# Kernel optimization log

Hardware: AMD Instinct MI355X
Metric: run time of the kernel (lower is better)

Reference implementation:

```python
import jax, jax.numpy as jnp
import numpy as np

N, S, R, M, C, CZ = 1, 128, 256, 256, 32, 128


def setup_inputs() -> dict:
    key = jax.random.key(0)
    k1, k2, k3, k4 = jax.random.split(key, 4)
    return {
        "msa_repr": jax.random.normal(k1, (N, S, R, M), dtype=jnp.float32) * 0.1,
        "left_w": jax.random.normal(k2, (M, C), dtype=jnp.float32) * 0.02,
        "right_w": jax.random.normal(k3, (M, C), dtype=jnp.float32) * 0.02,
        "out_w": jax.random.normal(k4, (C * C, CZ), dtype=jnp.float32) * 0.02,
    }


def reference(msa_repr, left_w, right_w, out_w):
    # msa_repr: [N,S,R,M]
    n, s, r, m = msa_repr.shape
    c = left_w.shape[1]
    # opm_projection: [N,S,R,M] @ [M,C] -> [N,S,R,C]
    left = jnp.einsum('nsrm,mc->nsrc', msa_repr, left_w)
    right = jnp.einsum('nsrm,mc->nsrc', msa_repr, right_w)
    # outer product summed over MSA dim s: [N,R,T,C,C]
    # (torch: a=left.transpose(-2,-3) -> [N,R,S,C]; einsum '...bac,...dae->...bdce')
    outer = jnp.einsum('nsrc,nste->nrtce', left, right).reshape(n, r, r, c * c)
    # project to pair channel: [N,R,T,C*C] @ [C*C,CZ] -> [N,R,T,CZ]
    return jnp.matmul(outer, out_w)
```

## Files before the change

kernel.cpp:

```cpp
#include <hip/hip_runtime.h>
#include <stdint.h>

#define S_DIM 128
#define R_DIM 256
#define M_DIM 256
#define C_DIM 32
#define CZ_DIM 128
#define K2_DIM 1024

typedef _Float16 f16;
typedef _Float16 f16x4 __attribute__((ext_vector_type(4)));
typedef _Float16 f16x8 __attribute__((ext_vector_type(8)));
typedef float f32x4 __attribute__((ext_vector_type(4)));
typedef float f32x16 __attribute__((ext_vector_type(16)));

typedef const __attribute__((address_space(1))) uint32_t gu32_t;
typedef __attribute__((address_space(3))) uint32_t lu32_t;
#define GLOAD_LDS16(g, l) \
    __builtin_amdgcn_global_load_lds((gu32_t*)(g), (lu32_t*)(l), 16, 0, 0)

__global__ __launch_bounds__(256, 4)
void proj_kernel(const float* __restrict__ msa, const float* __restrict__ lw,
                 const float* __restrict__ rw, const float* __restrict__ ow,
                 f16* __restrict__ left_t, f16* __restrict__ rt2,
                 f16* __restrict__ wt2) {
    __shared__ __align__(16) f16 wlT[8192];
    __shared__ __align__(16) f16 wrT[8192];

    int bid = blockIdx.x;
    int tid = threadIdx.x;
    int w = tid >> 6;
    int lane = tid & 63;
    int q = lane >> 4, li = lane & 15;
    int r  = bid >> 1;
    int s0 = (bid & 1) << 6;
    int s_col = s0 + w * 16 + li;

    const f32x4* bp = (const f32x4*)(msa + ((size_t)s_col * R_DIM + r) * M_DIM + q * 8);
    f32x4 b[16];
#pragma unroll
    for (int ks = 0; ks < 8; ks++) { b[2 * ks] = bp[ks * 8]; b[2 * ks + 1] = bp[ks * 8 + 1]; }

    {
        int i = bid * 256 + tid;
        int cz = i >> 10, k2 = i & 1023;
        int c = k2 >> 5, e = k2 & 31;
        int k2p = ((e >> 2) << 7) + (c << 2) + (e & 3);
        int ntile = cz >> 5, l31o = cz & 31;
        int kk = k2p >> 4, q5o = (k2p >> 3) & 1, j = k2p & 7;
        wt2[(ntile * 64 + kk) * 512 + (l31o * 2 + q5o) * 8 + j] = (f16)ow[k2 * CZ_DIM + cz];
    }
#pragma unroll
    for (int k = 0; k < 32; k++) {
        int i = k * 256 + tid;
        int m = i >> 5, c = i & 31;
        int d = ((m >> 3) * 32 + c) * 8 + (m & 7);
        wlT[d] = (f16)lw[i];
        wrT[d] = (f16)rw[i];
    }
    __syncthreads();

    f32x4 aL0 = {0,0,0,0}, aL1 = {0,0,0,0}, aR0 = {0,0,0,0}, aR1 = {0,0,0,0};
#pragma unroll
    for (int ks = 0; ks < 8; ks++) {
        f16x8 bf;
#pragma unroll
        for (int u = 0; u < 4; u++) { bf[u] = (f16)b[2*ks][u]; bf[4 + u] = (f16)b[2*ks+1][u]; }
        const f16* a0 = wlT + ((ks * 4 + q) * 32 + li) * 8;
        const f16* a1 = wrT + ((ks * 4 + q) * 32 + li) * 8;
        f16x8 al0 = *(const f16x8*)(a0);
        f16x8 al1 = *(const f16x8*)(a0 + 128);
        f16x8 ar0 = *(const f16x8*)(a1);
        f16x8 ar1 = *(const f16x8*)(a1 + 128);
        aL0 = __builtin_amdgcn_mfma_f32_16x16x32_f16(al0, bf, aL0, 0, 0, 0);
        aL1 = __builtin_amdgcn_mfma_f32_16x16x32_f16(al1, bf, aL1, 0, 0, 0);
        aR0 = __builtin_amdgcn_mfma_f32_16x16x32_f16(ar0, bf, aR0, 0, 0, 0);
        aR1 = __builtin_amdgcn_mfma_f32_16x16x32_f16(ar1, bf, aR1, 0, 0, 0);
    }
    int ks_s = s_col >> 4, q5_s = (s_col >> 3) & 1, j_s = s_col & 7;
    int sbase = (r * 8 + ks_s) * 512 + q5_s * 8 + j_s;
    int rl = r & 7;
    f16* Lb = left_t + (size_t)(r >> 3) * 32768;
    int sc = s_col >> 3, sj = s_col & 7;
#pragma unroll
    for (int reg = 0; reg < 4; reg++) {
        int c0 = q * 4 + reg;
        int row0 = rl * 32 + c0;
        int swz = sc ^ c0;
        Lb[(row0 * 16 + swz) * 8 + sj]        = (f16)aL0[reg];
        Lb[((row0 + 16) * 16 + swz) * 8 + sj] = (f16)aL1[reg];
        rt2[sbase + c0 * 16]        = (f16)aR0[reg];
        rt2[sbase + (c0 + 16) * 16] = (f16)aR1[reg];
    }
}

__global__ __launch_bounds__(512, 4)
void fuse_kernel(const f16* __restrict__ left_t, const f16* __restrict__ rt2,
                 const f16* __restrict__ wt2, float* __restrict__ out) {
    __shared__ __align__(16) char lds[65536];
    f16* Ls = (f16*)lds;

    int bid0 = blockIdx.x;
    int bid = (bid0 & 7) * 256 + (bid0 >> 3);
    int br = bid >> 6, bt = bid & 63;
    int tid = threadIdx.x;
    int w = tid >> 6, lane = tid & 63;
    int q5 = lane >> 5, l31 = lane & 31, lx = lane & 15;

    const f16* Lg = left_t + (size_t)br * 32768;

#pragma unroll
    for (int it = 0; it < 8; it++) {
        GLOAD_LDS16(Lg + (size_t)(it * 512 + tid) * 8, Ls + (it * 512 + tid) * 8);
    }

    int t_tile = w & 3, rg4 = w >> 2;
    int g = bt * 4 + t_tile;
    const f16* ap = rt2 + (size_t)g * 4096 + (l31 * 2 + q5) * 8;
    f16x8 afr[8];
#pragma unroll
    for (int ks = 0; ks < 8; ks++) afr[ks] = *(const f16x8*)(ap + ks * 512);

    __syncthreads();

    f32x16 acc[4] = {};
    __builtin_amdgcn_s_setprio(1);
#pragma unroll
    for (int i = 0; i < 4; i++) {
        const f16* bbase = Ls + ((rg4 * 4 + i) * 32 + l31) * 128;
#pragma unroll
        for (int ks = 0; ks < 8; ks++) {
            f16x8 bfr = *(const f16x8*)(bbase + (((2 * ks + q5) ^ lx) << 3));
            acc[i] = __builtin_amdgcn_mfma_f32_32x32x16_f16(afr[ks], bfr, acc[i], 0, 0, 0);
        }
    }
    __builtin_amdgcn_s_setprio(0);

    int ntile = w & 3, kh = w >> 2;
    const f16* wbase = wt2 + (size_t)(ntile * 64 + kh * 32) * 512 + (l31 * 2 + q5) * 8;
    f16x8 wfg[8][4];
#pragma unroll
    for (int u = 0; u < 4; u++) wfg[0][u] = *(const f16x8*)(wbase + u * 512);

    __syncthreads();

    int chc = l31 >> 1, bsub = 8 * (l31 & 1);
#pragma unroll
    for (int i = 0; i < 4; i++) {
        int p = (rg4 * 4 + i) * 4 + t_tile;
        char* prow = lds + p * 2048;
#pragma unroll
        for (int rg = 0; rg < 4; rg++) {
            int ch = (2 * rg + q5) * 16 + chc;
            int phys = (ch + p) & 127;
            f16x4 h = {(f16)acc[i][4 * rg], (f16)acc[i][4 * rg + 1],
                       (f16)acc[i][4 * rg + 2], (f16)acc[i][4 * rg + 3]};
            *(f16x4*)(prow + phys * 16 + bsub) = h;
        }
    }
    __syncthreads();

    const char* lbase = lds + l31 * 2048;
    int base = 64 * kh + q5 + l31;
    f16x8 afg[8][4];
    f32x16 accA = {}, accB = {};
    __builtin_amdgcn_s_setprio(1);
#pragma unroll
    for (int gg = 0; gg < 8; gg++) {
        if (gg == 0) {
#pragma unroll
            for (int u = 0; u < 4; u++) wfg[1][u] = *(const f16x8*)(wbase + (4 + u) * 512);
#pragma unroll
            for (int u = 0; u < 4; u++) wfg[2][u] = *(const f16x8*)(wbase + (8 + u) * 512);
#pragma unroll
            for (int u = 0; u < 4; u++)
                afg[0][u] = *(const f16x8*)(lbase + (((base + 2 * u) & 127) << 4));
#pragma unroll
            for (int u = 0; u < 4; u++)
                afg[1][u] = *(const f16x8*)(lbase + (((base + 8 + 2 * u) & 127) << 4));
        } else {
            if (gg + 2 < 8) {
#pragma unroll
                for (int u = 0; u < 4; u++)
                    wfg[gg + 2][u] = *(const f16x8*)(wbase + ((gg + 2) * 4 + u) * 512);
            }
            if (gg + 1 < 8) {
#pragma unroll
                for (int u = 0; u < 4; u++)
                    afg[gg + 1][u] = *(const f16x8*)(lbase + (((base + (gg + 1) * 8 + 2 * u) & 127) << 4));
            }
        }
        accA = __builtin_amdgcn_mfma_f32_32x32x16_f16(afg[gg][0], wfg[gg][0], accA, 0, 0, 0);
        accB = __builtin_amdgcn_mfma_f32_32x32x16_f16(afg[gg][1], wfg[gg][1], accB, 0, 0, 0);
        accA = __builtin_amdgcn_mfma_f32_32x32x16_f16(afg[gg][2], wfg[gg][2], accA, 0, 0, 0);
        accB = __builtin_amdgcn_mfma_f32_32x32x16_f16(afg[gg][3], wfg[gg][3], accB, 0, 0, 0);
    }
    __builtin_amdgcn_s_setprio(0);
    f32x16 acc2;
#pragma unroll
    for (int v = 0; v < 16; v++) acc2[v] = accA[v] + accB[v];
    __syncthreads();

    if (w >= 4) {
        char* rb = lds + (w - 4) * 4096 + lane * 64;
#pragma unroll
        for (int u = 0; u < 4; u++) {
            f32x4 part = {acc2[4 * u], acc2[4 * u + 1], acc2[4 * u + 2], acc2[4 * u + 3]};
            *(f32x4*)(rb + u * 16) = part;
        }
    }
    __syncthreads();
    if (w < 4) {
        const char* rb = lds + w * 4096 + lane * 64;
#pragma unroll
        for (int u = 0; u < 4; u++) {
            f32x4 part = *(const f32x4*)(rb + u * 16);
#pragma unroll
            for (int v = 0; v < 4; v++) acc2[4 * u + v] += part[v];
        }
        int r0 = br * 8, t0 = bt * 4, cz = w * 32 + l31;
#pragma unroll
        for (int reg = 0; reg < 16; reg++) {
            int p = (reg & 3) + 8 * (reg >> 2) + 4 * q5;
            out[((size_t)((r0 + (p >> 2)) * R_DIM + t0 + (p & 3))) * CZ_DIM + cz] = acc2[reg];
        }
    }
}

extern "C" void kernel_launch(void* const* d_in, const int* in_sizes, int n_in,
                              void* d_out, int out_size, void* d_ws, size_t ws_size,
                              hipStream_t stream) {
    const float* msa = (const float*)d_in[0];
    const float* lw  = (const float*)d_in[1];
    const float* rw  = (const float*)d_in[2];
    const float* ow  = (const float*)d_in[3];
    char* ws = (char*)d_ws;
    f16* left_t = (f16*)(ws);
    f16* rt2    = (f16*)(ws + (size_t)2 * 1024 * 1024);
    f16* wt2    = (f16*)(ws + (size_t)4 * 1024 * 1024);
    float* out  = (float*)d_out;

    proj_kernel<<<dim3(512), dim3(256), 0, stream>>>(msa, lw, rw, ow, left_t, rt2, wt2);
    fuse_kernel<<<dim3(2048), dim3(512), 0, stream>>>(left_t, rt2, wt2, out);
}
```

Before: 134.3 us.

## Split outer-product MFMA loop and interleave LDS stores with second half compute

```diff
diff --git a/kernel.cpp b/kernel.cpp
--- a/kernel.cpp
+++ b/kernel.cpp
@@ -121,12 +121,16 @@
 #pragma unroll
     for (int ks = 0; ks < 8; ks++) afr[ks] = *(const f16x8*)(ap + ks * 512);
 
+    int ntile = w & 3, kh = w >> 2;
+    const f16* wbase = wt2 + (size_t)(ntile * 64 + kh * 32) * 512 + (l31 * 2 + q5) * 8;
+    int chc = l31 >> 1, bsub = 8 * (l31 & 1);
+
     __syncthreads();
 
     f32x16 acc[4] = {};
     __builtin_amdgcn_s_setprio(1);
 #pragma unroll
-    for (int i = 0; i < 4; i++) {
+    for (int i = 0; i < 2; i++) {
         const f16* bbase = Ls + ((rg4 * 4 + i) * 32 + l31) * 128;
 #pragma unroll
         for (int ks = 0; ks < 8; ks++) {
@@ -136,17 +140,25 @@
     }
     __builtin_amdgcn_s_setprio(0);
 
-    int ntile = w & 3, kh = w >> 2;
-    const f16* wbase = wt2 + (size_t)(ntile * 64 + kh * 32) * 512 + (l31 * 2 + q5) * 8;
+    __syncthreads();
+
     f16x8 wfg[8][4];
 #pragma unroll
     for (int u = 0; u < 4; u++) wfg[0][u] = *(const f16x8*)(wbase + u * 512);
 
-    __syncthreads();
-
-    int chc = l31 >> 1, bsub = 8 * (l31 & 1);
-#pragma unroll
-    for (int i = 0; i < 4; i++) {
+    __builtin_amdgcn_s_setprio(1);
+#pragma unroll
+    for (int i = 2; i < 4; i++) {
+        const f16* bbase = Ls + ((rg4 * 4 + i) * 32 + l31) * 128;
+#pragma unroll
+        for (int ks = 0; ks < 8; ks++) {
+            f16x8 bfr = *(const f16x8*)(bbase + (((2 * ks + q5) ^ lx) << 3));
+            acc[i] = __builtin_amdgcn_mfma_f32_32x32x16_f16(afr[ks], bfr, acc[i], 0, 0, 0);
+        }
+    }
+    __builtin_amdgcn_s_setprio(0);
+#pragma unroll
+    for (int i = 0; i < 2; i++) {
         int p = (rg4 * 4 + i) * 4 + t_tile;
         char* prow = lds + p * 2048;
 #pragma unroll
@@ -158,37 +170,52 @@
             *(f16x4*)(prow + phys * 16 + bsub) = h;
         }
     }
+
+    __syncthreads();
+
+#pragma unroll
+    for (int s = 1; s < 4; s++) {
+#pragma unroll
+        for (int u = 0; u < 4; u++) wfg[s][u] = *(const f16x8*)(wbase + (s * 4 + u) * 512);
+    }
+#pragma unroll
+    for (int i = 2; i < 4; i++) {
+        int p = (rg4 * 4 + i) * 4 + t_tile;
+        char* prow = lds + p * 2048;
+#pragma unroll
+        for (int rg = 0; rg < 4; rg++) {
+            int ch = (2 * rg + q5) * 16 + chc;
+            int phys = (ch + p) & 127;
+            f16x4 h = {(f16)acc[i][4 * rg], (f16)acc[i][4 * rg + 1],
+                       (f16)acc[i][4 * rg + 2], (f16)acc[i][4 * rg + 3]};
+            *(f16x4*)(prow + phys * 16 + bsub) = h;
+        }
+    }
     __syncthreads();
 
     const char* lbase = lds + l31 * 2048;
     int base = 64 * kh + q5 + l31;
     f16x8 afg[8][4];
     f32x16 accA = {}, accB = {};
+#pragma unroll
+    for (int u = 0; u < 4; u++)
+        afg[0][u] = *(const f16x8*)(lbase + (((base + 2 * u) & 127) << 4));
+#pragma unroll
+    for (int u = 0; u < 4; u++)
+        afg[1][u] = *(const f16x8*)(lbase + (((base + 8 + 2 * u) & 127) << 4));
+
     __builtin_amdgcn_s_setprio(1);
 #pragma unroll
     for (int gg = 0; gg < 8; gg++) {
-        if (gg == 0) {
-#pragma unroll
-            for (int u = 0; u < 4; u++) wfg[1][u] = *(const f16x8*)(wbase + (4 + u) * 512);
-#pragma unroll
-            for (int u = 0; u < 4; u++) wfg[2][u] = *(const f16x8*)(wbase + (8 + u) * 512);
+        if (gg + 4 < 8) {
 #pragma unroll
             for (int u = 0; u < 4; u++)
-                afg[0][u] = *(const f16x8*)(lbase + (((base + 2 * u) & 127) << 4));
+                wfg[gg + 4][u] = *(const f16x8*)(wbase + ((gg + 4) * 4 + u) * 512);
+        }
+        if (gg >= 1 && gg + 1 < 8) {
 #pragma unroll
             for (int u = 0; u < 4; u++)
-                afg[1][u] = *(const f16x8*)(lbase + (((base + 8 + 2 * u) & 127) << 4));
-        } else {
-            if (gg + 2 < 8) {
-#pragma unroll
-                for (int u = 0; u < 4; u++)
-                    wfg[gg + 2][u] = *(const f16x8*)(wbase + ((gg + 2) * 4 + u) * 512);
-            }
-            if (gg + 1 < 8) {
-#pragma unroll
-                for (int u = 0; u < 4; u++)
-                    afg[gg + 1][u] = *(const f16x8*)(lbase + (((base + (gg + 1) * 8 + 2 * u) & 127) << 4));
-            }
+                afg[gg + 1][u] = *(const f16x8*)(lbase + (((base + (gg + 1) * 8 + 2 * u) & 127) << 4));
         }
         accA = __builtin_amdgcn_mfma_f32_32x32x16_f16(afg[gg][0], wfg[gg][0], accA, 0, 0, 0);
         accB = __builtin_amdgcn_mfma_f32_32x32x16_f16(afg[gg][1], wfg[gg][1], accB, 0, 0, 0);
```

Result: no change. 136.3 us (+1.5%).
